# Kernel optimization log

Measured on AMD Instinct MI355X. Metric: run time of the kernel, lower is better.

The kernel has to match this reference:

```python
import jax, jax.numpy as jnp
import numpy as np

B, PLEN, D = 32, 1024, 256


def setup_inputs() -> dict:
    key = jax.random.key(0)
    ks = jax.random.split(key, 8)
    u = lambda k, shape: jax.random.uniform(k, shape, jnp.float32, -0.05, 0.05)
    return {
        "P": jax.random.normal(ks[0], (B, PLEN, D), jnp.float32),
        "w_itr_att": u(ks[1], (3 * D,)),
        "w1": u(ks[2], (2 * D, D)),
        "w2": u(ks[3], (2 * D, D)),
        "w3": u(ks[4], (2 * D, D)),
        "b1": u(ks[5], (D,)),
        "b2": u(ks[6], (D,)),
        "b3": u(ks[7], (D,)),
    }


def reference(P, w_itr_att, w1, w2, w3, b1, b2, b3):
    d = P.shape[-1]
    # alpha(a,b) = w_itr_att . [a ; b ; a*b]; split w into the three d-chunks
    wa, wb, wc = w_itr_att[:d], w_itr_att[d:2 * d], w_itr_att[2 * d:]
    # pairwise score A[b,i,j] = wa.P_i + wb.P_j + wc.(P_i * P_j)
    sa = P @ wa                                   # (b, p)
    sb = P @ wb                                   # (b, p)
    A = sa[:, :, None] + sb[:, None, :] + jnp.einsum('bid,bjd->bij', P * wc, P)
    itr_attn = jnp.einsum('bij,bjd->bid', jax.nn.softmax(A, axis=2), P)
    cat = jnp.concatenate([P, itr_attn], axis=-1)  # (b, p, 2d)
    z = jnp.tanh(cat @ w1 + b1)
    r = jax.nn.sigmoid(cat @ w2 + b2)
    f = jax.nn.sigmoid(cat @ w3 + b3)
    return r * P + f * z
```

## Files before the change

### kernel.cpp

```cpp
#include <hip/hip_runtime.h>
#include <hip/hip_bf16.h>

typedef unsigned short u16;
typedef unsigned int   u32;
typedef unsigned char  u8;

using bf16x8 = __attribute__((ext_vector_type(8))) short;
using f32x4  = __attribute__((ext_vector_type(4))) float;

#define NB 32
#define NP 1024
#define ND 256

__device__ __forceinline__ u16 f2bf(float x){
  u32 u = __float_as_uint(x);
  u += 0x7FFFu + ((u >> 16) & 1u);
  return (u16)(u >> 16);
}

__device__ __forceinline__ float bf2f(u16 x){
  return __uint_as_float((u32)x << 16);
}

__device__ __forceinline__ u8 f2e4m3(float x){
  u32 b = __float_as_uint(x);
  u32 s = (b >> 31) << 7;
  float ax = __uint_as_float(b & 0x7fffffffu);
  if (!(ax < 464.f)) return (u8)(s | 0x7E);
  if (ax < 0.001953125f) return (u8)s;
  if (ax < 0.015625f){
    u32 m = (u32)__float2int_rn(ax * 512.f);
    return (u8)(s | m);
  }
  u32 bb = b & 0x7fffffffu;
  bb += 0x7ffffu + ((bb >> 20) & 1u);
  int e = (int)(bb >> 23) - 127 + 7;
  u32 m = (bb >> 20) & 7u;
  if (e > 15 || (e == 15 && m == 7)) return (u8)(s | 0x7E);
  return (u8)(s | ((u32)e << 3) | m);
}
#if __has_builtin(__builtin_amdgcn_cvt_pk_fp8_f32)
template<bool HI>
__device__ __forceinline__ u32 pk_fp8(float a, float b, u32 old){
  return (u32)__builtin_amdgcn_cvt_pk_fp8_f32(a, b, (int)old, HI);
}
__device__ __forceinline__ u8 f8byte(float x){
  return (u8)(pk_fp8<false>(x, 0.f, 0) & 0xFFu);
}
#else
template<bool HI>
__device__ __forceinline__ u32 pk_fp8(float a, float b, u32 old){
  u32 v = (u32)f2e4m3(a) | ((u32)f2e4m3(b) << 8);
  return HI ? ((old & 0xFFFFu) | (v << 16)) : ((old & 0xFFFF0000u) | v);
}
__device__ __forceinline__ u8 f8byte(float x){ return f2e4m3(x); }
#endif

__device__ __forceinline__ void glds16(const void* g, void* l){
  __builtin_amdgcn_global_load_lds((const __attribute__((address_space(1))) void*)g,
                                   (__attribute__((address_space(3))) void*)l, 16, 0, 0);
}

__global__ void prep_pt(const float* __restrict__ P, const float* __restrict__ wi,
                        u16* __restrict__ Pbf, u16* __restrict__ PbfT,
                        u8* __restrict__ P8, float* __restrict__ sbv){
  const int b = blockIdx.y, jt = blockIdx.x;
  __shared__ __align__(16) u16 T[64][264];
  const int tid = threadIdx.x;
  const int row = tid >> 2;
  const int dq  = tid & 3;
  const size_t grow = (size_t)b * NP + jt * 64 + row;
  const float* prow = P + grow * ND;
  const float* wbp  = wi + ND;
  float s = 0.f;
  #pragma unroll
  for (int it = 0; it < 4; ++it){
    const int d0 = it * 64 + dq * 16;
    float4 a0 = *(const float4*)(prow + d0);
    float4 a1 = *(const float4*)(prow + d0 + 4);
    float4 a2 = *(const float4*)(prow + d0 + 8);
    float4 a3 = *(const float4*)(prow + d0 + 12);
    float4 w0 = *(const float4*)(wbp + d0);
    float4 w1 = *(const float4*)(wbp + d0 + 4);
    float4 w2 = *(const float4*)(wbp + d0 + 8);
    float4 w3 = *(const float4*)(wbp + d0 + 12);
    s += a0.x*w0.x + a0.y*w0.y + a0.z*w0.z + a0.w*w0.w;
    s += a1.x*w1.x + a1.y*w1.y + a1.z*w1.z + a1.w*w1.w;
    s += a2.x*w2.x + a2.y*w2.y + a2.z*w2.z + a2.w*w2.w;
    s += a3.x*w3.x + a3.y*w3.y + a3.z*w3.z + a3.w*w3.w;
    u16 tmp[16];
    tmp[0]=f2bf(a0.x); tmp[1]=f2bf(a0.y); tmp[2]=f2bf(a0.z); tmp[3]=f2bf(a0.w);
    tmp[4]=f2bf(a1.x); tmp[5]=f2bf(a1.y); tmp[6]=f2bf(a1.z); tmp[7]=f2bf(a1.w);
    tmp[8]=f2bf(a2.x); tmp[9]=f2bf(a2.y); tmp[10]=f2bf(a2.z); tmp[11]=f2bf(a2.w);
    tmp[12]=f2bf(a3.x); tmp[13]=f2bf(a3.y); tmp[14]=f2bf(a3.z); tmp[15]=f2bf(a3.w);
    *(uint4*)&T[row][d0]     = *(uint4*)tmp;
    *(uint4*)&T[row][d0 + 8] = *(uint4*)(tmp + 8);
    *(uint4*)(Pbf + grow * ND + d0)     = *(uint4*)tmp;
    *(uint4*)(Pbf + grow * ND + d0 + 8) = *(uint4*)(tmp + 8);
    u32 q0 = pk_fp8<false>(a0.x, a0.y, 0); q0 = pk_fp8<true>(a0.z, a0.w, q0);
    u32 q1 = pk_fp8<false>(a1.x, a1.y, 0); q1 = pk_fp8<true>(a1.z, a1.w, q1);
    u32 q2 = pk_fp8<false>(a2.x, a2.y, 0); q2 = pk_fp8<true>(a2.z, a2.w, q2);
    u32 q3 = pk_fp8<false>(a3.x, a3.y, 0); q3 = pk_fp8<true>(a3.z, a3.w, q3);
    uint4 pq; pq.x = q0; pq.y = q1; pq.z = q2; pq.w = q3;
    *(uint4*)(P8 + grow * ND + d0) = pq;
  }
  s += __shfl_xor(s, 1, 64);
  s += __shfl_xor(s, 2, 64);
  if (dq == 0) sbv[grow] = s;
  __syncthreads();
  #pragma unroll
  for (int it = 0; it < 8; ++it){
    int cc = tid + 256 * it;
    int d = cc >> 3, c8 = cc & 7;
    u16 tmp[8];
    #pragma unroll
    for (int k = 0; k < 8; ++k) tmp[k] = T[c8 * 8 + k][d];
    *(uint4*)(PbfT + ((size_t)b * ND + d) * NP + jt * 64 + c8 * 8) = *(uint4*)tmp;
  }
}

__global__ void prep_w(const float* __restrict__ w1, const float* __restrict__ w2,
                       const float* __restrict__ w3,
                       u16* __restrict__ Wp, u8* __restrict__ W8){
  const int t = blockIdx.x;
  const float* w = (t < 16) ? w1 : ((t < 32) ? w2 : w3);
  const int tid = threadIdx.x;
  #pragma unroll
  for (int j = 0; j < 4; ++j){
    int item = tid + 256 * j;
    int c = item >> 6, lane = item & 63;
    int ncol = ((t & 15) << 4) + (lane & 15);
    int k0 = 32 * c + 8 * (lane >> 4);
    if (c < 8){
      u16 tmp[8];
      #pragma unroll
      for (int e = 0; e < 8; ++e) tmp[e] = f2bf(w[(size_t)(k0 + e) * 256 + ncol]);
      *(uint4*)(Wp + ((size_t)(t * 8 + c) * 64 + lane) * 8) = *(uint4*)tmp;
    } else {
      u32 lo32 = pk_fp8<false>(16.f * w[(size_t)(k0+0)*256+ncol], 16.f * w[(size_t)(k0+1)*256+ncol], 0);
      lo32     = pk_fp8<true >(16.f * w[(size_t)(k0+2)*256+ncol], 16.f * w[(size_t)(k0+3)*256+ncol], lo32);
      u32 hi32 = pk_fp8<false>(16.f * w[(size_t)(k0+4)*256+ncol], 16.f * w[(size_t)(k0+5)*256+ncol], 0);
      hi32     = pk_fp8<true >(16.f * w[(size_t)(k0+6)*256+ncol], 16.f * w[(size_t)(k0+7)*256+ncol], hi32);
      uint2 pv; pv.x = lo32; pv.y = hi32;
      *(uint2*)(W8 + ((size_t)(t * 8 + (c - 8)) * 64 + lane) * 8) = pv;
    }
  }
}

__launch_bounds__(256, 2)
__global__ void attn_kernel(const float* __restrict__ P, const float* __restrict__ wi,
                            const u8* __restrict__ P8, const u16* __restrict__ PbfT,
                            const float* __restrict__ sbv, u8* __restrict__ attnb8){
  const int p    = blockIdx.x;
  const int bid  = ((p & 7) << 6) | (p >> 3);
  const int b    = bid >> 4;
  const int q0   = (bid & 15) << 6;
  const int tid  = threadIdx.x;
  const int wave = tid >> 6, lane = tid & 63, lo = lane & 15, hi = lane >> 4;

  __shared__ __align__(16) u8  Kt8[64 * 256];
  __shared__ __align__(16) u16 VtA[256 * 64];
  __shared__ __align__(16) u16 Sp[4][16][72];
  __shared__ float sls[4][16];
  __shared__ float lfin[64];
  __shared__ u32 fastf[4];
  char* KtB = (char*)Kt8;
  char* VtB = (char*)VtA;

  long qf8[8];
  {
    const int qrow = q0 + wave * 16 + lo;
    const float* prow = P  + ((size_t)b * NP + qrow) * ND;
    const float* wcp  = wi + 512;
    #pragma unroll
    for (int c = 0; c < 8; ++c){
      const int d0 = 32 * c + 8 * hi;
      float4 a  = *(const float4*)(prow + d0);
      float4 a2 = *(const float4*)(prow + d0 + 4);
      float4 wa  = *(const float4*)(wcp + d0);
      float4 wa2 = *(const float4*)(wcp + d0 + 4);
      u32 w0 = pk_fp8<false>(16.f*a.x*wa.x,  16.f*a.y*wa.y,  0);
      w0     = pk_fp8<true >(16.f*a.z*wa.z,  16.f*a.w*wa.w,  w0);
      u32 w1 = pk_fp8<false>(16.f*a2.x*wa2.x, 16.f*a2.y*wa2.y, 0);
      w1     = pk_fp8<true >(16.f*a2.z*wa2.z, 16.f*a2.w*wa2.w, w1);
      qf8[c] = (long)(((unsigned long long)w1 << 32) | w0);
    }
  }

  f32x4 of[4][4];
  #pragma unroll
  for (int qt = 0; qt < 4; ++qt)
    #pragma unroll
    for (int dt = 0; dt < 4; ++dt) of[qt][dt] = (f32x4){0.f,0.f,0.f,0.f};
  float mx[4] = {-1e30f,-1e30f,-1e30f,-1e30f};
  float ls[4] = {0.f,0.f,0.f,0.f};

  const u8*  kslab = P8   + (size_t)b * NP * ND;
  const u16* vslab = PbfT + (size_t)b * ND * NP;

  auto stageK = [&](int kt){
    const int kbase = kt * 64;
    #pragma unroll
    for (int it = 0; it < 4; ++it){
      int off = it * 4096 + tid * 16;
      int j   = off >> 8;
      int u   = ((off >> 4) & 15) ^ (j & 7);
      glds16((const char*)(kslab + (size_t)(kbase + j) * ND + u * 16), KtB + off);
    }
  };
  auto stageV = [&](int kt){
    const int kbase = kt * 64;
    #pragma unroll
    for (int it = 0; it < 8; ++it){
      int off = it * 4096 + tid * 16;
      int d   = off >> 7;
      int kc  = ((off >> 4) & 7) ^ (d & 7);
      glds16((const char*)(vslab + (size_t)d * NP + kbase + kc * 8), VtB + off);
    }
  };

  float sbc[4], sbn[4];
  stageK(0);
  stageV(0);
  #pragma unroll
  for (int nt = 0; nt < 4; ++nt) sbc[nt] = sbv[(size_t)b * NP + nt * 16 + lo];
  __syncthreads();

  for (int kt = 0; kt < 16; ++kt){
    f32x4 s[4];
    #pragma unroll
    for (int nt = 0; nt < 4; ++nt){
      f32x4 acc = (f32x4){0.f,0.f,0.f,0.f};
      #pragma unroll
      for (int c = 0; c < 8; ++c){
        int j  = nt * 16 + lo;
        int ad = j * 256 + (((2 * c + (hi >> 1)) ^ (j & 7)) << 4) + 8 * (hi & 1);
        long kf8 = *(const long*)(KtB + ad);
        acc = __builtin_amdgcn_mfma_f32_16x16x32_fp8_fp8(qf8[c], kf8, acc, 0, 0, 0);
      }
      float sv = sbc[nt];
      #pragma unroll
      for (int r = 0; r < 4; ++r) s[nt][r] = fmaf(acc[r], 0.0625f, sv);
    }

    float scale[4] = {1.f, 1.f, 1.f, 1.f};
    int fast = 1;
    {
      float md = -1e30f;
      #pragma unroll
      for (int nt = 0; nt < 4; ++nt)
        #pragma unroll
        for (int r = 0; r < 4; ++r) md = fmaxf(md, s[nt][r] - mx[r]);
      if (!__all(md <= 8.f)){
        fast = 0;
        #pragma unroll
        for (int r = 0; r < 4; ++r){
          float v = fmaxf(fmaxf(s[0][r], s[1][r]), fmaxf(s[2][r], s[3][r]));
          v = fmaxf(v, __shfl_xor(v, 1, 64));
          v = fmaxf(v, __shfl_xor(v, 2, 64));
          v = fmaxf(v, __shfl_xor(v, 4, 64));
          v = fmaxf(v, __shfl_xor(v, 8, 64));
          float mnew = fmaxf(mx[r], v);
          scale[r] = __expf(mx[r] - mnew);
          mx[r] = mnew;
          ls[r] *= scale[r];
        }
      }
    }
    #pragma unroll
    for (int nt = 0; nt < 4; ++nt)
      #pragma unroll
      for (int r = 0; r < 4; ++r){
        float pv = __expf(s[nt][r] - mx[r]);
        ls[r] += pv;
        Sp[wave][4 * hi + r][16 * nt + lo] = f2bf(pv);
      }
    if (lane == 0) fastf[wave] = (u32)fast;
    if (lo == 0){
      #pragma unroll
      for (int r = 0; r < 4; ++r) sls[wave][4 * hi + r] = scale[r];
    }

    __syncthreads();
    if (kt < 15) stageK(kt + 1);

    if (!(fastf[0] & fastf[1] & fastf[2] & fastf[3])){
      #pragma unroll
      for (int qt = 0; qt < 4; ++qt){
        #pragma unroll
        for (int r = 0; r < 4; ++r){
          float sc = sls[qt][4 * hi + r];
          #pragma unroll
          for (int dt = 0; dt < 4; ++dt) of[qt][dt][r] *= sc;
        }
      }
    }

    #pragma unroll
    for (int kk = 0; kk < 2; ++kk){
      bf16x8 pa[4];
      #pragma unroll
      for (int qt = 0; qt < 4; ++qt)
        pa[qt] = *(const bf16x8*)&Sp[qt][lo][32 * kk + 8 * hi];
      #pragma unroll
      for (int dt = 0; dt < 4; ++dt){
        int d  = wave * 64 + dt * 16 + lo;
        int ad = d * 128 + (((4 * kk + hi) ^ (d & 7)) << 4);
        bf16x8 vb = *(const bf16x8*)(VtB + ad);
        #pragma unroll
        for (int qt = 0; qt < 4; ++qt)
          of[qt][dt] = __builtin_amdgcn_mfma_f32_16x16x32_bf16(pa[qt], vb, of[qt][dt], 0, 0, 0);
      }
    }

    __syncthreads();
    if (kt < 15){
      stageV(kt + 1);
      #pragma unroll
      for (int nt = 0; nt < 4; ++nt)
        sbn[nt] = sbv[(size_t)b * NP + (kt + 1) * 64 + nt * 16 + lo];
      sbc[0] = sbn[0]; sbc[1] = sbn[1]; sbc[2] = sbn[2]; sbc[3] = sbn[3];
    }
  }

  #pragma unroll
  for (int r = 0; r < 4; ++r){
    ls[r] += __shfl_xor(ls[r], 1, 64);
    ls[r] += __shfl_xor(ls[r], 2, 64);
    ls[r] += __shfl_xor(ls[r], 4, 64);
    ls[r] += __shfl_xor(ls[r], 8, 64);
  }
  if (lo == 0){
    #pragma unroll
    for (int r = 0; r < 4; ++r) lfin[wave * 16 + 4 * hi + r] = ls[r];
  }
  __syncthreads();
  #pragma unroll
  for (int qt = 0; qt < 4; ++qt){
    #pragma unroll
    for (int r = 0; r < 4; ++r){
      const float inv = 1.f / lfin[qt * 16 + 4 * hi + r];
      const int qrow = q0 + qt * 16 + 4 * hi + r;
      #pragma unroll
      for (int dt = 0; dt < 4; ++dt){
        float o = of[qt][dt][r] * inv;
        attnb8[((size_t)b * NP + qrow) * ND + wave * 64 + dt * 16 + lo] = f8byte(o);
      }
    }
  }
}

__launch_bounds__(256, 2)
__global__ void mlp_kernel(const u16* __restrict__ Pbf, const u8* __restrict__ attnb8,
                           const u16* __restrict__ Wp, const u8* __restrict__ W8,
                           const float* __restrict__ Pf,
                           const float* __restrict__ b1, const float* __restrict__ b2,
                           const float* __restrict__ b3, float* __restrict__ out){
  const int p    = blockIdx.x;
  const int swz  = ((p & 7) << 7) | (p >> 3);
  const int mt   = swz >> 2, cg = swz & 3;
  const int tid  = threadIdx.x;
  const int wave = tid >> 6, lane = tid & 63, lo = lane & 15, hi = lane >> 4;
  const int tq   = 4 * cg + wave;
  const int m0   = mt * 128;

  __shared__ __align__(16) u16 Ab16[2][128 * 64];
  __shared__ __align__(16) u8  Ab8[2][128 * 64];

  f32x4 acc[3][8];
  #pragma unroll
  for (int e = 0; e < 3; ++e)
    #pragma unroll
    for (int m = 0; m < 8; ++m) acc[e][m] = (f32x4){0.f,0.f,0.f,0.f};

  auto stage16 = [&](int s, int buf){
    const u16* xs = Pbf + (size_t)m0 * ND + s * 64;
    char* dst = (char*)Ab16[buf];
    #pragma unroll
    for (int it = 0; it < 4; ++it){
      int off = it * 4096 + tid * 16;
      int row = off >> 7;
      int cl  = (off & 127) ^ ((row & 7) << 4);
      glds16((const char*)(xs + (size_t)row * ND) + cl, dst + off);
    }
  };
  auto stage8 = [&](int s, int buf){
    const u8* xs = attnb8 + (size_t)m0 * ND + s * 64;
    char* dst = (char*)Ab8[buf];
    #pragma unroll
    for (int it = 0; it < 2; ++it){
      int off = it * 4096 + tid * 16;
      int row = off >> 6;
      int u   = ((off >> 4) & 3) ^ ((row >> 1) & 3);
      glds16((const char*)(xs + (size_t)row * ND + u * 16), dst + off);
    }
  };

  stage8(0, 0);
  __syncthreads();
  for (int s = 0; s < 4; ++s){
    if (s < 3) stage8(s + 1, (s + 1) & 1);
    else       stage16(0, 0);
    const char* ab = (const char*)Ab8[s & 1];
    #pragma unroll
    for (int cc = 0; cc < 2; ++cc){
      const int c = 2 * s + cc;
      long wf8[3];
      #pragma unroll
      for (int e = 0; e < 3; ++e)
        wf8[e] = *(const long*)(W8 + ((size_t)((tq + 16 * e) * 8 + c) * 64 + lane) * 8);
      #pragma unroll
      for (int m = 0; m < 8; ++m){
        int row = 16 * m + lo;
        int ad  = row * 64 + (((2 * cc + (hi >> 1)) ^ ((row >> 1) & 3)) << 4) + 8 * (hi & 1);
        long af8 = *(const long*)(ab + ad);
        #pragma unroll
        for (int e = 0; e < 3; ++e)
          acc[e][m] = __builtin_amdgcn_mfma_f32_16x16x32_fp8_fp8(af8, wf8[e], acc[e][m], 0, 0, 0);
      }
    }
    __syncthreads();
  }

  #pragma unroll
  for (int e = 0; e < 3; ++e)
    #pragma unroll
    for (int m = 0; m < 8; ++m)
      #pragma unroll
      for (int r = 0; r < 4; ++r) acc[e][m][r] *= 0.0625f;

  for (int s = 0; s < 4; ++s){
    if (s < 3) stage16(s + 1, (s + 1) & 1);
    const char* ab = (const char*)Ab16[s & 1];
    #pragma unroll
    for (int cc = 0; cc < 2; ++cc){
      const int c = 2 * s + cc;
      bf16x8 wf[3];
      #pragma unroll
      for (int e = 0; e < 3; ++e)
        wf[e] = *(const bf16x8*)(Wp + ((size_t)((tq + 16 * e) * 8 + c) * 64 + lane) * 8);
      #pragma unroll
      for (int m = 0; m < 8; ++m){
        int row = 16 * m + lo;
        bf16x8 af = *(const bf16x8*)(ab + row * 128 + ((64 * cc + 16 * hi) ^ ((row & 7) << 4)));
        #pragma unroll
        for (int e = 0; e < 3; ++e)
          acc[e][m] = __builtin_amdgcn_mfma_f32_16x16x32_bf16(af, wf[e], acc[e][m], 0, 0, 0);
      }
    }
    __syncthreads();
  }

  const int d = 16 * tq + lo;
  const float bb1 = b1[d], bb2 = b2[d], bb3 = b3[d];
  #pragma unroll
  for (int m = 0; m < 8; ++m){
    #pragma unroll
    for (int r = 0; r < 4; ++r){
      const int row = m0 + 16 * m + 4 * hi + r;
      float y1 = acc[0][m][r] + bb1;
      float y2 = acc[1][m][r] + bb2;
      float y3 = acc[2][m][r] + bb3;
      float pv = Pf[(size_t)row * ND + d];
      float e2 = __expf(2.f * y1);
      float z  = (e2 - 1.f) / (e2 + 1.f);
      float rr = 1.f / (1.f + __expf(-y2));
      float ff = 1.f / (1.f + __expf(-y3));
      out[(size_t)row * ND + d] = rr * pv + ff * z;
    }
  }
}

extern "C" void kernel_launch(void* const* d_in, const int* in_sizes, int n_in,
                              void* d_out, int out_size, void* d_ws, size_t ws_size,
                              hipStream_t stream){
  const float* P  = (const float*)d_in[0];
  const float* wi = (const float*)d_in[1];
  const float* w1 = (const float*)d_in[2];
  const float* w2 = (const float*)d_in[3];
  const float* w3 = (const float*)d_in[4];
  const float* b1 = (const float*)d_in[5];
  const float* b2 = (const float*)d_in[6];
  const float* b3 = (const float*)d_in[7];
  float* out = (float*)d_out;

  char* ws = (char*)d_ws;
  u16*   PbfT  = (u16*)  (ws);
  u8*    P8    = (u8*)   (ws + (16u << 20));
  u8*    atn8  = (u8*)   (ws + (24u << 20));
  u16*   Pbf   = (u16*)  (ws + (32u << 20));
  u16*   Wp    = (u16*)  (ws + (48u << 20));
  u8*    W8    = (u8*)   (ws + (48u << 20) + 524288);
  float* sbv   = (float*)(ws + (49u << 20));

  prep_pt<<<dim3(16, 32), 256, 0, stream>>>(P, wi, Pbf, PbfT, P8, sbv);
  prep_w<<<48, 256, 0, stream>>>(w1, w2, w3, Wp, W8);
  attn_kernel<<<512, 256, 0, stream>>>(P, wi, P8, PbfT, sbv, atn8);
  mlp_kernel<<<1024, 256, 0, stream>>>(Pbf, atn8, Wp, W8, P, b1, b2, b3, out);
}
```

Baseline: 109.1 us.

## Switch attention PV matmul to FP8 with FP8 transposed V and probabilities

The transposed V copy is now stored as FP8 instead of bf16, and softmax probabilities are scaled by 1/8 and written as FP8. This lets the PV product use the fp8 MFMA, halves V staging traffic and shrinks LDS, with the scale undone in the final normalisation. The MLP epilogue also reads the bf16 copy of P instead of the fp32 input, cutting residual read bandwidth. The cost is lower precision in both the attention output and the residual term.

```diff
diff --git a/kernel.cpp b/kernel.cpp
--- a/kernel.cpp
+++ b/kernel.cpp
@@ -62,7 +62,7 @@
 }
 
 __global__ void prep_pt(const float* __restrict__ P, const float* __restrict__ wi,
-                        u16* __restrict__ Pbf, u16* __restrict__ PbfT,
+                        u16* __restrict__ Pbf, u8* __restrict__ PT8,
                         u8* __restrict__ P8, float* __restrict__ sbv){
   const int b = blockIdx.y, jt = blockIdx.x;
   __shared__ __align__(16) u16 T[64][264];
@@ -112,10 +112,14 @@
   for (int it = 0; it < 8; ++it){
     int cc = tid + 256 * it;
     int d = cc >> 3, c8 = cc & 7;
-    u16 tmp[8];
-    #pragma unroll
-    for (int k = 0; k < 8; ++k) tmp[k] = T[c8 * 8 + k][d];
-    *(uint4*)(PbfT + ((size_t)b * ND + d) * NP + jt * 64 + c8 * 8) = *(uint4*)tmp;
+    float v0 = bf2f(T[c8 * 8 + 0][d]), v1 = bf2f(T[c8 * 8 + 1][d]);
+    float v2 = bf2f(T[c8 * 8 + 2][d]), v3 = bf2f(T[c8 * 8 + 3][d]);
+    float v4 = bf2f(T[c8 * 8 + 4][d]), v5 = bf2f(T[c8 * 8 + 5][d]);
+    float v6 = bf2f(T[c8 * 8 + 6][d]), v7 = bf2f(T[c8 * 8 + 7][d]);
+    u32 lo32 = pk_fp8<false>(v0, v1, 0); lo32 = pk_fp8<true>(v2, v3, lo32);
+    u32 hi32 = pk_fp8<false>(v4, v5, 0); hi32 = pk_fp8<true>(v6, v7, hi32);
+    uint2 pv; pv.x = lo32; pv.y = hi32;
+    *(uint2*)(PT8 + ((size_t)b * ND + d) * NP + jt * 64 + c8 * 8) = pv;
   }
 }
 
@@ -149,7 +153,7 @@
 
 __launch_bounds__(256, 2)
 __global__ void attn_kernel(const float* __restrict__ P, const float* __restrict__ wi,
-                            const u8* __restrict__ P8, const u16* __restrict__ PbfT,
+                            const u8* __restrict__ P8, const u8* __restrict__ PT8,
                             const float* __restrict__ sbv, u8* __restrict__ attnb8){
   const int p    = blockIdx.x;
   const int bid  = ((p & 7) << 6) | (p >> 3);
@@ -159,13 +163,13 @@
   const int wave = tid >> 6, lane = tid & 63, lo = lane & 15, hi = lane >> 4;
 
   __shared__ __align__(16) u8  Kt8[64 * 256];
-  __shared__ __align__(16) u16 VtA[256 * 64];
-  __shared__ __align__(16) u16 Sp[4][16][72];
+  __shared__ __align__(16) u8  Vt8[256 * 64];
+  __shared__ __align__(16) u8  Sp8[4][16][80];
   __shared__ float sls[4][16];
   __shared__ float lfin[64];
   __shared__ u32 fastf[4];
   char* KtB = (char*)Kt8;
-  char* VtB = (char*)VtA;
+  char* VtB = (char*)Vt8;
 
   long qf8[8];
   {
@@ -195,8 +199,8 @@
   float mx[4] = {-1e30f,-1e30f,-1e30f,-1e30f};
   float ls[4] = {0.f,0.f,0.f,0.f};
 
-  const u8*  kslab = P8   + (size_t)b * NP * ND;
-  const u16* vslab = PbfT + (size_t)b * ND * NP;
+  const u8* kslab = P8  + (size_t)b * NP * ND;
+  const u8* vslab = PT8 + (size_t)b * ND * NP;
 
   auto stageK = [&](int kt){
     const int kbase = kt * 64;
@@ -211,11 +215,12 @@
   auto stageV = [&](int kt){
     const int kbase = kt * 64;
     #pragma unroll
-    for (int it = 0; it < 8; ++it){
+    for (int it = 0; it < 4; ++it){
       int off = it * 4096 + tid * 16;
-      int d   = off >> 7;
-      int kc  = ((off >> 4) & 7) ^ (d & 7);
-      glds16((const char*)(vslab + (size_t)d * NP + kbase + kc * 8), VtB + off);
+      int d   = off >> 6;
+      int t   = (off >> 4) & 3;
+      int u   = t ^ ((d >> 1) & 3);
+      glds16((const char*)(vslab + (size_t)d * NP + kbase + u * 16), VtB + off);
     }
   };
 
@@ -273,7 +278,7 @@
       for (int r = 0; r < 4; ++r){
         float pv = __expf(s[nt][r] - mx[r]);
         ls[r] += pv;
-        Sp[wave][4 * hi + r][16 * nt + lo] = f2bf(pv);
+        Sp8[wave][4 * hi + r][16 * nt + lo] = f8byte(pv * 0.125f);
       }
     if (lane == 0) fastf[wave] = (u32)fast;
     if (lo == 0){
@@ -298,18 +303,18 @@
 
     #pragma unroll
     for (int kk = 0; kk < 2; ++kk){
-      bf16x8 pa[4];
+      long pa8[4];
       #pragma unroll
       for (int qt = 0; qt < 4; ++qt)
-        pa[qt] = *(const bf16x8*)&Sp[qt][lo][32 * kk + 8 * hi];
+        pa8[qt] = *(const long*)&Sp8[qt][lo][32 * kk + 8 * hi];
       #pragma unroll
       for (int dt = 0; dt < 4; ++dt){
         int d  = wave * 64 + dt * 16 + lo;
-        int ad = d * 128 + (((4 * kk + hi) ^ (d & 7)) << 4);
-        bf16x8 vb = *(const bf16x8*)(VtB + ad);
+        int ad = d * 64 + (((4 * kk + hi) ^ (d & 6)) << 3);
+        long vb8 = *(const long*)(VtB + ad);
         #pragma unroll
         for (int qt = 0; qt < 4; ++qt)
-          of[qt][dt] = __builtin_amdgcn_mfma_f32_16x16x32_bf16(pa[qt], vb, of[qt][dt], 0, 0, 0);
+          of[qt][dt] = __builtin_amdgcn_mfma_f32_16x16x32_fp8_fp8(pa8[qt], vb8, of[qt][dt], 0, 0, 0);
       }
     }
 
@@ -339,7 +344,7 @@
   for (int qt = 0; qt < 4; ++qt){
     #pragma unroll
     for (int r = 0; r < 4; ++r){
-      const float inv = 1.f / lfin[qt * 16 + 4 * hi + r];
+      const float inv = 8.f / lfin[qt * 16 + 4 * hi + r];
       const int qrow = q0 + qt * 16 + 4 * hi + r;
       #pragma unroll
       for (int dt = 0; dt < 4; ++dt){
@@ -353,7 +358,6 @@
 __launch_bounds__(256, 2)
 __global__ void mlp_kernel(const u16* __restrict__ Pbf, const u8* __restrict__ attnb8,
                            const u16* __restrict__ Wp, const u8* __restrict__ W8,
-                           const float* __restrict__ Pf,
                            const float* __restrict__ b1, const float* __restrict__ b2,
                            const float* __restrict__ b3, float* __restrict__ out){
   const int p    = blockIdx.x;
@@ -461,7 +465,7 @@
       float y1 = acc[0][m][r] + bb1;
       float y2 = acc[1][m][r] + bb2;
       float y3 = acc[2][m][r] + bb3;
-      float pv = Pf[(size_t)row * ND + d];
+      float pv = bf2f(Pbf[(size_t)row * ND + d]);
       float e2 = __expf(2.f * y1);
       float z  = (e2 - 1.f) / (e2 + 1.f);
       float rr = 1.f / (1.f + __expf(-y2));
@@ -485,16 +489,16 @@
   float* out = (float*)d_out;
 
   char* ws = (char*)d_ws;
-  u16*   PbfT  = (u16*)  (ws);
-  u8*    P8    = (u8*)   (ws + (16u << 20));
-  u8*    atn8  = (u8*)   (ws + (24u << 20));
-  u16*   Pbf   = (u16*)  (ws + (32u << 20));
-  u16*   Wp    = (u16*)  (ws + (48u << 20));
-  u8*    W8    = (u8*)   (ws + (48u << 20) + 524288);
-  float* sbv   = (float*)(ws + (49u << 20));
-
-  prep_pt<<<dim3(16, 32), 256, 0, stream>>>(P, wi, Pbf, PbfT, P8, sbv);
+  u8*    PT8   = (u8*)   (ws);
+  u8*    P8    = (u8*)   (ws + ( 8u << 20));
+  u8*    atn8  = (u8*)   (ws + (16u << 20));
+  u16*   Pbf   = (u16*)  (ws + (24u << 20));
+  u16*   Wp    = (u16*)  (ws + (40u << 20));
+  u8*    W8    = (u8*)   (ws + (40u << 20) + 524288);
+  float* sbv   = (float*)(ws + (41u << 20));
+
+  prep_pt<<<dim3(16, 32), 256, 0, stream>>>(P, wi, Pbf, PT8, P8, sbv);
   prep_w<<<48, 256, 0, stream>>>(w1, w2, w3, Wp, W8);
-  attn_kernel<<<512, 256, 0, stream>>>(P, wi, P8, PbfT, sbv, atn8);
-  mlp_kernel<<<1024, 256, 0, stream>>>(Pbf, atn8, Wp, W8, P, b1, b2, b3, out);
-}
+  attn_kernel<<<512, 256, 0, stream>>>(P, wi, P8, PT8, sbv, atn8);
+  mlp_kernel<<<1024, 256, 0, stream>>>(Pbf, atn8, Wp, W8, b1, b2, b3, out);
+}
```

After: 106.8 us. 1.02x faster.
